# Performance work log

Measured on AMD Instinct MI355X. Metric: run time of the kernel, lower is better.

## Reference

```python
import jax, jax.numpy as jnp
import numpy as np

NT, NH, NW = 16, 16, 16
HEADS, DIM_HEAD = 8, 64
DIM = 512
DEPTH = 4
EPS = 1e-5


def _layernorm(x, g, b):
    mu = jnp.mean(x, axis=-1, keepdims=True)
    var = jnp.mean(jnp.square(x - mu), axis=-1, keepdims=True)
    return (x - mu) * jax.lax.rsqrt(var + EPS) * g + b


def setup_inputs() -> dict:
    key = jax.random.key(0)
    ks = jax.random.split(key, 4)
    n = NT * NH * NW
    inner = HEADS * DIM_HEAD
    x = jax.random.normal(ks[0], (8, n, DIM), dtype=jnp.float32)
    Wqkv = jax.random.normal(ks[1], (DEPTH, DIM, 3 * inner), dtype=jnp.float32) * (DIM ** -0.5)
    Wout = jax.random.normal(ks[2], (DEPTH, inner, DIM), dtype=jnp.float32) * (inner ** -0.5)
    bout = jnp.zeros((DEPTH, DIM), dtype=jnp.float32)
    gamma = jnp.ones((DEPTH, DIM), dtype=jnp.float32)
    beta = jnp.zeros((DEPTH, DIM), dtype=jnp.float32)
    return {"x": x, "Wqkv": Wqkv, "Wout": Wout, "bout": bout, "gamma": gamma, "beta": beta}


def _fda_layer(x, Wqkv, Wout, bout, g, bb):
    b, n, d = x.shape
    hs = HEADS // 2
    s = NH * NW
    scale = DIM_HEAD ** -0.5
    y = _layernorm(x, g, bb)
    qkv = y @ Wqkv  # (b, n, 3*inner)
    q, k, v = jnp.split(qkv, 3, axis=-1)
    # b n (h d) -> b h n d
    def to_heads(t):
        return t.reshape(b, n, HEADS, DIM_HEAD).transpose(0, 2, 1, 3)
    q, k, v = to_heads(q), to_heads(k), to_heads(v)
    # spatial branch: first half of heads, view n as (t, s)
    qs = q[:, :hs].reshape(b, hs, NT, s, DIM_HEAD)
    ks = k[:, :hs].reshape(b, hs, NT, s, DIM_HEAD)
    vs = v[:, :hs].reshape(b, hs, NT, s, DIM_HEAD)
    sp_dots = jnp.einsum('bhtid,bhtjd->bhtij', qs, ks) * scale
    sp_attn = jax.nn.softmax(sp_dots, axis=-1)
    sp_out = jnp.einsum('bhtij,bhtjd->bhtid', sp_attn, vs)  # (b,hs,nt,s,dh)
    # temporal branch: second half of heads, view n as (s, t)
    qt = q[:, hs:].reshape(b, hs, s, NT, DIM_HEAD)
    kt = k[:, hs:].reshape(b, hs, s, NT, DIM_HEAD)
    vt = v[:, hs:].reshape(b, hs, s, NT, DIM_HEAD)
    tp_dots = jnp.einsum('bhsid,bhsjd->bhsij', qt, kt) * scale
    tp_attn = jax.nn.softmax(tp_dots, axis=-1)
    tp_out = jnp.einsum('bhsij,bhsjd->bhsid', tp_attn, vt)  # (b,hs,s,nt,dh)
    out = jnp.concatenate([sp_out.reshape(b, hs, n, DIM_HEAD),
                           tp_out.reshape(b, hs, n, DIM_HEAD)], axis=1)  # (b,h,n,dh)
    out = out.transpose(0, 2, 1, 3).reshape(b, n, HEADS * DIM_HEAD)
    return out @ Wout + bout


def reference(x, Wqkv, Wout, bout, gamma, beta):
    for l in range(DEPTH):
        x = _fda_layer(x, Wqkv[l], Wout[l], bout[l], gamma[l], beta[l]) + x
    return x
```

## Files before the change

kernel.cpp:

```cpp
#include <hip/hip_runtime.h>
#include <hip/hip_bf16.h>

typedef __bf16 bf16x8 __attribute__((ext_vector_type(8)));
typedef float f32x4 __attribute__((ext_vector_type(4)));

#define AS1(p) ((const __attribute__((address_space(1))) void*)(p))
#define AS3(p) ((__attribute__((address_space(3))) void*)(p))

__global__ __launch_bounds__(256) void transpose32(const float* __restrict__ W,
                                                   __bf16* __restrict__ WT,
                                                   int K, int N) {
  __shared__ float t[32][33];
  int l = blockIdx.z;
  int k0 = blockIdx.y * 32, n0 = blockIdx.x * 32;
  int tx = threadIdx.x & 31, ty = threadIdx.x >> 5;
  const float* src = W + ((size_t)l * K + k0) * N + n0;
#pragma unroll
  for (int i = 0; i < 32; i += 8) t[ty + i][tx] = src[(size_t)(ty + i) * N + tx];
  __syncthreads();
  __bf16* dst = WT + ((size_t)l * N + n0) * K + k0;
#pragma unroll
  for (int i = 0; i < 32; i += 8) dst[(size_t)(ty + i) * K + tx] = (__bf16)t[tx][ty + i];
}

__global__ __launch_bounds__(256) void ln_kernel(const float* __restrict__ x,
                                                 const float* __restrict__ gamma,
                                                 const float* __restrict__ beta,
                                                 __bf16* __restrict__ y) {
  int wave = threadIdx.x >> 6, lane = threadIdx.x & 63;
  size_t row = (size_t)blockIdx.x * 4 + wave;
  const float* xr = x + row * 512 + lane * 8;
  float4 v0 = *(const float4*)xr;
  float4 v1 = *(const float4*)(xr + 4);
  float s = v0.x + v0.y + v0.z + v0.w + v1.x + v1.y + v1.z + v1.w;
  float ss = v0.x * v0.x + v0.y * v0.y + v0.z * v0.z + v0.w * v0.w +
             v1.x * v1.x + v1.y * v1.y + v1.z * v1.z + v1.w * v1.w;
#pragma unroll
  for (int m = 1; m < 64; m <<= 1) {
    s += __shfl_xor(s, m);
    ss += __shfl_xor(ss, m);
  }
  float mean = s * (1.f / 512.f);
  float var = ss * (1.f / 512.f) - mean * mean;
  float rstd = rsqrtf(var + 1e-5f);
  const float* gp = gamma + lane * 8;
  const float* bp = beta + lane * 8;
  float4 g0 = *(const float4*)gp, g1 = *(const float4*)(gp + 4);
  float4 b0 = *(const float4*)bp, b1 = *(const float4*)(bp + 4);
  bf16x8 o;
  o[0] = (__bf16)((v0.x - mean) * rstd * g0.x + b0.x);
  o[1] = (__bf16)((v0.y - mean) * rstd * g0.y + b0.y);
  o[2] = (__bf16)((v0.z - mean) * rstd * g0.z + b0.z);
  o[3] = (__bf16)((v0.w - mean) * rstd * g0.w + b0.w);
  o[4] = (__bf16)((v1.x - mean) * rstd * g1.x + b1.x);
  o[5] = (__bf16)((v1.y - mean) * rstd * g1.y + b1.y);
  o[6] = (__bf16)((v1.z - mean) * rstd * g1.z + b1.z);
  o[7] = (__bf16)((v1.w - mean) * rstd * g1.w + b1.w);
  *(bf16x8*)(y + row * 512 + lane * 8) = o;
}

#define STAGE_PART(kt_, part_)                                                   \
  {                                                                              \
    const __bf16* gb_ = ((part_) < 2) ? Abase : Bbase;                           \
    int rowoff_ = ((part_)&1) * 128;                                             \
    const __bf16* g0_ = gb_ + (size_t)(rowoff_ + r0s) * 512 + (kt_)*64 + s0 * 8; \
    const __bf16* g1_ = gb_ + (size_t)(rowoff_ + r1s) * 512 + (kt_)*64 + s1 * 8; \
    char* lb_ = lds + (((kt_)&1) * 65536) + ((part_)*16384);                     \
    __builtin_amdgcn_global_load_lds(AS1(g0_), AS3(lb_ + ldsw0), 16, 0, 0);      \
    __builtin_amdgcn_global_load_lds(AS1(g1_), AS3(lb_ + ldsw1), 16, 0, 0);      \
  }

template <int NCOLS>
__global__ __launch_bounds__(512, 2) void gemm256(const __bf16* __restrict__ A,
                                                  const __bf16* __restrict__ BT,
                                                  __bf16* __restrict__ Cb) {
  extern __shared__ __attribute__((aligned(128))) char lds[];
  constexpr int NT = NCOLS / 256;
  int bid = blockIdx.x;
  int cpx = gridDim.x >> 3;
  int L = (bid & 7) * cpx + (bid >> 3);
  int tileM = L / NT, tileN = L - tileM * NT;
  int tid = threadIdx.x;
  int l = tid & 63, w = tid >> 6;
  int lm = l & 15, lh = l >> 4;
  int wave_m = w >> 2, wave_n = w & 3;
  const __bf16* Abase = A + (size_t)tileM * 256 * 512;
  const __bf16* Bbase = BT + (size_t)tileN * 256 * 512;
  int r0s = tid >> 3, s0 = (tid & 7) ^ (r0s & 7);
  int p1 = tid + 512;
  int r1s = p1 >> 3, s1 = (p1 & 7) ^ (r1s & 7);
  int ldsw0 = (w * 64) * 16, ldsw1 = (512 + w * 64) * 16;

  f32x4 acc[8][4];
#pragma unroll
  for (int m = 0; m < 8; ++m)
#pragma unroll
    for (int n = 0; n < 4; ++n) acc[m][n] = (f32x4){0.f, 0.f, 0.f, 0.f};

  int xorv = (lm & 7) << 4;
  int kb0 = (lh * 16) ^ xorv;
  int kb1 = (64 + lh * 16) ^ xorv;
  int arow = wave_m * 128 + lm;
  int brow = wave_n * 64 + lm;

  STAGE_PART(0, 0); STAGE_PART(0, 1); STAGE_PART(0, 2); STAGE_PART(0, 3);

  for (int kt = 0; kt < 8; ++kt) {
    char* sb = lds + (kt & 1) * 65536;
    if (kt < 7) {
      STAGE_PART(kt + 1, 0);
      asm volatile("s_waitcnt vmcnt(2)" ::: "memory");
    } else {
      asm volatile("s_waitcnt vmcnt(0)" ::: "memory");
    }
    __builtin_amdgcn_sched_barrier(0);
    __builtin_amdgcn_s_barrier();
    bf16x8 bfrag[4][2];
#pragma unroll
    for (int nf = 0; nf < 4; ++nf) {
      const char* bp = sb + 32768 + (brow + nf * 16) * 128;
      bfrag[nf][0] = *(const bf16x8*)(bp + kb0);
      bfrag[nf][1] = *(const bf16x8*)(bp + kb1);
    }
#pragma unroll
    for (int ph = 0; ph < 4; ++ph) {
      bf16x8 af[2][2];
#pragma unroll
      for (int m = 0; m < 2; ++m) {
        const char* ap = sb + (arow + (ph * 2 + m) * 16) * 128;
        af[m][0] = *(const bf16x8*)(ap + kb0);
        af[m][1] = *(const bf16x8*)(ap + kb1);
      }
      if (ph == 0 && kt < 7) STAGE_PART(kt + 1, 1);
      if (ph == 1 && kt < 7) STAGE_PART(kt + 1, 2);
      if (ph == 2 && kt < 7) STAGE_PART(kt + 1, 3);
      __builtin_amdgcn_s_setprio(1);
#pragma unroll
      for (int m = 0; m < 2; ++m)
#pragma unroll
        for (int nf = 0; nf < 4; ++nf) {
          acc[ph * 2 + m][nf] = __builtin_amdgcn_mfma_f32_16x16x32_bf16(
              af[m][0], bfrag[nf][0], acc[ph * 2 + m][nf], 0, 0, 0);
          acc[ph * 2 + m][nf] = __builtin_amdgcn_mfma_f32_16x16x32_bf16(
              af[m][1], bfrag[nf][1], acc[ph * 2 + m][nf], 0, 0, 0);
        }
      __builtin_amdgcn_s_setprio(0);
    }
    __builtin_amdgcn_s_barrier();
  }

  __syncthreads();
  __bf16* lw = (__bf16*)(lds + w * 9216);
  int crow0 = tileM * 256 + wave_m * 128;
  int ccol = tileN * 256 + wave_n * 64 + (l & 7) * 8;
#pragma unroll
  for (int half = 0; half < 2; ++half) {
#pragma unroll
    for (int m2 = 0; m2 < 4; ++m2) {
      int mf = half * 4 + m2;
#pragma unroll
      for (int nf = 0; nf < 4; ++nf)
#pragma unroll
        for (int r = 0; r < 4; ++r)
          lw[(m2 * 16 + lh * 4 + r) * 72 + nf * 16 + lm] = (__bf16)acc[mf][nf][r];
    }
    asm volatile("s_waitcnt lgkmcnt(0)" ::: "memory");
    __builtin_amdgcn_sched_barrier(0);
#pragma unroll
    for (int p = 0; p < 8; ++p) {
      int lrow = p * 8 + (l >> 3);
      bf16x8 v = *(const bf16x8*)&lw[lrow * 72 + (l & 7) * 8];
      *(bf16x8*)&Cb[(size_t)(crow0 + half * 64 + lrow) * NCOLS + ccol] = v;
    }
    asm volatile("s_waitcnt lgkmcnt(0)" ::: "memory");
    __builtin_amdgcn_sched_barrier(0);
  }
}

#define STAGE_SB(kt_)                                                            \
  {                                                                              \
    const __bf16* gA0_ = Abase + (size_t)rA0 * 512 + (kt_)*64 + sA0 * 8;         \
    const __bf16* gA1_ = Abase + (size_t)rA1 * 512 + (kt_)*64 + sA1 * 8;         \
    __builtin_amdgcn_global_load_lds(AS1(gA0_), AS3(lds + dW0), 16, 0, 0);       \
    __builtin_amdgcn_global_load_lds(AS1(gA1_), AS3(lds + 8192 + dW0), 16, 0, 0);\
    __builtin_amdgcn_global_load_lds(AS1(Bbase + (size_t)rA0 * 512 + (kt_)*64 + sA0 * 8), \
                                     AS3(lds + 16384 + dW0), 16, 0, 0);          \
    __builtin_amdgcn_global_load_lds(AS1(Bbase + (size_t)rA1 * 512 + (kt_)*64 + sA1 * 8), \
                                     AS3(lds + 24576 + dW0), 16, 0, 0);          \
    __builtin_amdgcn_global_load_lds(AS1(Bbase + (size_t)(128 + rA0) * 512 + (kt_)*64 + sA0 * 8), \
                                     AS3(lds + 32768 + dW0), 16, 0, 0);          \
    __builtin_amdgcn_global_load_lds(AS1(Bbase + (size_t)(128 + rA1) * 512 + (kt_)*64 + sA1 * 8), \
                                     AS3(lds + 40960 + dW0), 16, 0, 0);          \
  }

__global__ __launch_bounds__(512) void gemm_sb(const __bf16* __restrict__ A,
                                               const __bf16* __restrict__ BT,
                                               __bf16* __restrict__ Cb) {
  extern __shared__ __attribute__((aligned(128))) char lds[];
  constexpr int NCOLS = 1536;
  constexpr int NT = 6;
  int bid = blockIdx.x;
  int cpx = gridDim.x >> 3;
  int L = (bid & 7) * cpx + (bid >> 3);
  int tileM = L / NT, tileN = L - tileM * NT;
  int tid = threadIdx.x;
  int l = tid & 63, w = tid >> 6;
  int lm = l & 15, lh = l >> 4;
  int wave_m = w >> 2, wave_n = w & 3;
  const __bf16* Abase = A + (size_t)tileM * 128 * 512;
  const __bf16* Bbase = BT + (size_t)tileN * 256 * 512;
  int rA0 = tid >> 3, sA0 = (tid & 7) ^ (rA0 & 7);
  int p1 = tid + 512;
  int rA1 = p1 >> 3, sA1 = (p1 & 7) ^ (rA1 & 7);
  int dW0 = w * 1024;

  f32x4 acc[4][4];
#pragma unroll
  for (int m = 0; m < 4; ++m)
#pragma unroll
    for (int n = 0; n < 4; ++n) acc[m][n] = (f32x4){0.f, 0.f, 0.f, 0.f};

  int xorv = (lm & 7) << 4;
  int kb0 = (lh * 16) ^ xorv;
  int kb1 = (64 + lh * 16) ^ xorv;
  int arow = wave_m * 64 + lm;
  int brow = wave_n * 64 + lm;

  STAGE_SB(0);
  asm volatile("s_waitcnt vmcnt(0)" ::: "memory");
  __builtin_amdgcn_sched_barrier(0);
  __builtin_amdgcn_s_barrier();

  for (int kt = 0; kt < 8; ++kt) {
    bf16x8 bfrag[4][2];
#pragma unroll
    for (int nf = 0; nf < 4; ++nf) {
      const char* bp = lds + 16384 + (brow + nf * 16) * 128;
      bfrag[nf][0] = *(const bf16x8*)(bp + kb0);
      bfrag[nf][1] = *(const bf16x8*)(bp + kb1);
    }
    __builtin_amdgcn_s_setprio(1);
#pragma unroll
    for (int mf = 0; mf < 4; ++mf) {
      const char* ap = lds + (arow + mf * 16) * 128;
      bf16x8 af0 = *(const bf16x8*)(ap + kb0);
      bf16x8 af1 = *(const bf16x8*)(ap + kb1);
#pragma unroll
      for (int nf = 0; nf < 4; ++nf) {
        acc[mf][nf] = __builtin_amdgcn_mfma_f32_16x16x32_bf16(af0, bfrag[nf][0],
                                                              acc[mf][nf], 0, 0, 0);
        acc[mf][nf] = __builtin_amdgcn_mfma_f32_16x16x32_bf16(af1, bfrag[nf][1],
                                                              acc[mf][nf], 0, 0, 0);
      }
    }
    __builtin_amdgcn_s_setprio(0);
    asm volatile("s_waitcnt lgkmcnt(0)" ::: "memory");
    __builtin_amdgcn_sched_barrier(0);
    __builtin_amdgcn_s_barrier();
    if (kt < 7) {
      STAGE_SB(kt + 1);
      asm volatile("s_waitcnt vmcnt(0)" ::: "memory");
      __builtin_amdgcn_sched_barrier(0);
      __builtin_amdgcn_s_barrier();
    }
  }

  __syncthreads();
  __bf16* lw = (__bf16*)(lds + w * 4608);
  int crow0 = tileM * 128 + wave_m * 64;
  int ccol = tileN * 256 + wave_n * 64 + (l & 7) * 8;
#pragma unroll
  for (int half = 0; half < 2; ++half) {
#pragma unroll
    for (int m2 = 0; m2 < 2; ++m2) {
      int mf = half * 2 + m2;
#pragma unroll
      for (int nf = 0; nf < 4; ++nf)
#pragma unroll
        for (int r = 0; r < 4; ++r)
          lw[(m2 * 16 + lh * 4 + r) * 72 + nf * 16 + lm] = (__bf16)acc[mf][nf][r];
    }
    asm volatile("s_waitcnt lgkmcnt(0)" ::: "memory");
    __builtin_amdgcn_sched_barrier(0);
#pragma unroll
    for (int p = 0; p < 4; ++p) {
      int lrow = p * 8 + (l >> 3);
      bf16x8 v = *(const bf16x8*)&lw[lrow * 72 + (l & 7) * 8];
      *(bf16x8*)&Cb[(size_t)(crow0 + half * 32 + lrow) * NCOLS + ccol] = v;
    }
    asm volatile("s_waitcnt lgkmcnt(0)" ::: "memory");
    __builtin_amdgcn_sched_barrier(0);
  }
}

#define STAGE128(kt_, part_)                                                    \
  {                                                                             \
    const __bf16* gb_ = ((part_) == 0) ? Abase : Bbase;                         \
    const __bf16* g0_ = gb_ + (size_t)r0s * 512 + (kt_)*64 + s0 * 8;            \
    const __bf16* g1_ = gb_ + (size_t)r1s * 512 + (kt_)*64 + s1 * 8;            \
    char* lb_ = lds + (((kt_)&1) * 32768) + ((part_)*16384);                    \
    __builtin_amdgcn_global_load_lds(AS1(g0_), AS3(lb_ + ldsw0), 16, 0, 0);     \
    __builtin_amdgcn_global_load_lds(AS1(g1_), AS3(lb_ + ldsw1), 16, 0, 0);     \
  }

__global__ __launch_bounds__(512, 4) void gemm128res(const __bf16* __restrict__ A,
                                                     const __bf16* __restrict__ BT,
                                                     float* Cf,
                                                     const float* __restrict__ bias,
                                                     const float* Resid) {
  extern __shared__ __attribute__((aligned(128))) char lds[];
  constexpr int NCOLS = 512;
  constexpr int NT = 4;
  int bid = blockIdx.x;
  int cpx = gridDim.x >> 3;
  int L = (bid & 7) * cpx + (bid >> 3);
  int tileM = L / NT, tileN = L - tileM * NT;
  int tid = threadIdx.x;
  int l = tid & 63, w = tid >> 6;
  int lm = l & 15, lh = l >> 4;
  int wave_m = w >> 2, wave_n = w & 3;
  const __bf16* Abase = A + (size_t)tileM * 128 * 512;
  const __bf16* Bbase = BT + (size_t)tileN * 128 * 512;
  int r0s = tid >> 3, s0 = (tid & 7) ^ (r0s & 7);
  int p1 = tid + 512;
  int r1s = p1 >> 3, s1 = (p1 & 7) ^ (r1s & 7);
  int ldsw0 = (w * 64) * 16, ldsw1 = 8192 + (w * 64) * 16;

  f32x4 acc[4][2];
#pragma unroll
  for (int m = 0; m < 4; ++m)
#pragma unroll
    for (int n = 0; n < 2; ++n) acc[m][n] = (f32x4){0.f, 0.f, 0.f, 0.f};

  int xorv = (lm & 7) << 4;
  int kb0 = (lh * 16) ^ xorv;
  int kb1 = (64 + lh * 16) ^ xorv;
  int arow = wave_m * 64 + lm;
  int brow = wave_n * 32 + lm;

  STAGE128(0, 0); STAGE128(0, 1);

  for (int kt = 0; kt < 8; ++kt) {
    char* sb = lds + (kt & 1) * 32768;
    if (kt < 7) {
      STAGE128(kt + 1, 0);
      asm volatile("s_waitcnt vmcnt(2)" ::: "memory");
    } else {
      asm volatile("s_waitcnt vmcnt(0)" ::: "memory");
    }
    __builtin_amdgcn_sched_barrier(0);
    __builtin_amdgcn_s_barrier();
    bf16x8 bfrag[2][2];
#pragma unroll
    for (int nf = 0; nf < 2; ++nf) {
      const char* bp = sb + 16384 + (brow + nf * 16) * 128;
      bfrag[nf][0] = *(const bf16x8*)(bp + kb0);
      bfrag[nf][1] = *(const bf16x8*)(bp + kb1);
    }
    bf16x8 af[4][2];
#pragma unroll
    for (int mf = 0; mf < 4; ++mf) {
      const char* ap = sb + (arow + mf * 16) * 128;
      af[mf][0] = *(const bf16x8*)(ap + kb0);
      af[mf][1] = *(const bf16x8*)(ap + kb1);
    }
    if (kt < 7) STAGE128(kt + 1, 1);
    __builtin_amdgcn_s_setprio(1);
#pragma unroll
    for (int mf = 0; mf < 4; ++mf)
#pragma unroll
      for (int nf = 0; nf < 2; ++nf) {
        acc[mf][nf] = __builtin_amdgcn_mfma_f32_16x16x32_bf16(af[mf][0], bfrag[nf][0],
                                                              acc[mf][nf], 0, 0, 0);
        acc[mf][nf] = __builtin_amdgcn_mfma_f32_16x16x32_bf16(af[mf][1], bfrag[nf][1],
                                                              acc[mf][nf], 0, 0, 0);
      }
    __builtin_amdgcn_s_setprio(0);
    __builtin_amdgcn_s_barrier();
  }

  float* lf = (float*)(lds + w * 2560);
  int crow0 = tileM * 128 + wave_m * 64;
  int ccol0 = tileN * 128 + wave_n * 32;
  int erow = l >> 2;
  int ecl = (l & 3) * 8;
  float4 ba = *(const float4*)(bias + ccol0 + ecl);
  float4 bb = *(const float4*)(bias + ccol0 + ecl + 4);
#pragma unroll
  for (int mf = 0; mf < 4; ++mf) {
#pragma unroll
    for (int nf = 0; nf < 2; ++nf)
#pragma unroll
      for (int r = 0; r < 4; ++r)
        lf[(lh * 4 + r) * 40 + nf * 16 + lm] = acc[mf][nf][r];
    size_t rowg = (size_t)(crow0 + mf * 16 + erow);
    const float* rp = Resid + rowg * NCOLS + ccol0 + ecl;
    float* cp = Cf + rowg * NCOLS + ccol0 + ecl;
    float4 a0 = *(float4*)&lf[erow * 40 + ecl];
    float4 a1 = *(float4*)&lf[erow * 40 + ecl + 4];
    float4 r0 = *(const float4*)rp;
    float4 r1 = *(const float4*)(rp + 4);
    float4 o0, o1;
    o0.x = a0.x + ba.x + r0.x; o0.y = a0.y + ba.y + r0.y;
    o0.z = a0.z + ba.z + r0.z; o0.w = a0.w + ba.w + r0.w;
    o1.x = a1.x + bb.x + r1.x; o1.y = a1.y + bb.y + r1.y;
    o1.z = a1.z + bb.z + r1.z; o1.w = a1.w + bb.w + r1.w;
    *(float4*)cp = o0;
    *(float4*)(cp + 4) = o1;
  }
}

__global__ __launch_bounds__(256) void attn_spatial(const __bf16* __restrict__ qkv,
                                                    __bf16* __restrict__ attn_out) {
  __shared__ __attribute__((aligned(16))) __bf16 VT[64 * 256];
  __shared__ __attribute__((aligned(16))) __bf16 P[4][4096];
  int bid = blockIdx.x;
  int b = bid >> 6;
  int rem = bid & 63;
  int h = rem >> 4;
  int t = rem & 15;
  int tid = threadIdx.x;
  int w = tid >> 6, l = tid & 63;
  size_t nbase = (size_t)b * 4096 + t * 256;
#pragma unroll
  for (int i = 0; i < 8; i++) {
    int idx = tid + i * 256;
    int key = idx >> 3, dseg = idx & 7;
    bf16x8 v = *(const bf16x8*)(qkv + (nbase + key) * 1536 + 1024 + h * 64 + dseg * 8);
#pragma unroll
    for (int d2 = 0; d2 < 8; d2++) {
      int dh = dseg * 8 + d2;
      VT[dh * 256 + (((key >> 3) ^ (dh & 7)) << 3) + (key & 7)] = v[d2];
    }
  }
  __syncthreads();
  int lm = l & 15, lh = l >> 4;
  for (int it = 0; it < 4; ++it) {
    int qbase = it * 64 + w * 16;
    const __bf16* qp = qkv + (nbase + qbase + lm) * 1536 + h * 64 + lh * 8;
    bf16x8 aq0 = *(const bf16x8*)qp;
    bf16x8 aq1 = *(const bf16x8*)(qp + 32);
    f32x4 sa[16];
#pragma unroll
    for (int tn = 0; tn < 16; ++tn) {
      const __bf16* kp = qkv + (nbase + tn * 16 + lm) * 1536 + 512 + h * 64 + lh * 8;
      bf16x8 bk0 = *(const bf16x8*)kp;
      bf16x8 bk1 = *(const bf16x8*)(kp + 32);
      f32x4 z = {0.f, 0.f, 0.f, 0.f};
      z = __builtin_amdgcn_mfma_f32_16x16x32_bf16(aq0, bk0, z, 0, 0, 0);
      sa[tn] = __builtin_amdgcn_mfma_f32_16x16x32_bf16(aq1, bk1, z, 0, 0, 0);
    }
    float rmax[4] = {-1e30f, -1e30f, -1e30f, -1e30f};
#pragma unroll
    for (int tn = 0; tn < 16; ++tn)
#pragma unroll
      for (int r = 0; r < 4; ++r) {
        sa[tn][r] *= 0.125f;
        rmax[r] = fmaxf(rmax[r], sa[tn][r]);
      }
#pragma unroll
    for (int m = 1; m < 16; m <<= 1)
#pragma unroll
      for (int r = 0; r < 4; ++r) rmax[r] = fmaxf(rmax[r], __shfl_xor(rmax[r], m));
    float rsum[4] = {0.f, 0.f, 0.f, 0.f};
#pragma unroll
    for (int tn = 0; tn < 16; ++tn)
#pragma unroll
      for (int r = 0; r < 4; ++r) {
        float e = __expf(sa[tn][r] - rmax[r]);
        sa[tn][r] = e;
        rsum[r] += e;
      }
#pragma unroll
    for (int m = 1; m < 16; m <<= 1)
#pragma unroll
      for (int r = 0; r < 4; ++r) rsum[r] += __shfl_xor(rsum[r], m);
    float rinv[4];
#pragma unroll
    for (int r = 0; r < 4; ++r) rinv[r] = 1.f / rsum[r];
#pragma unroll
    for (int tn = 0; tn < 16; ++tn)
#pragma unroll
      for (int r = 0; r < 4; ++r) {
        int row = lh * 4 + r;
        int col = tn * 16 + lm;
        P[w][row * 256 + ((((col >> 3)) ^ (row & 7)) << 3) + (col & 7)] =
            (__bf16)(sa[tn][r] * rinv[r]);
      }
    f32x4 oa[4];
#pragma unroll
    for (int nt = 0; nt < 4; ++nt) oa[nt] = (f32x4){0.f, 0.f, 0.f, 0.f};
#pragma unroll
    for (int kc = 0; kc < 8; ++kc) {
      bf16x8 pa = *(const bf16x8*)&P[w][lm * 256 + (((kc * 4 + lh) ^ (lm & 7)) << 3)];
#pragma unroll
      for (int nt = 0; nt < 4; ++nt) {
        int dh = nt * 16 + lm;
        bf16x8 bv = *(const bf16x8*)&VT[dh * 256 + (((kc * 4 + lh) ^ (dh & 7)) << 3)];
        oa[nt] = __builtin_amdgcn_mfma_f32_16x16x32_bf16(pa, bv, oa[nt], 0, 0, 0);
      }
    }
#pragma unroll
    for (int nt = 0; nt < 4; ++nt)
#pragma unroll
      for (int r = 0; r < 4; ++r) {
        size_t row = nbase + qbase + lh * 4 + r;
        attn_out[row * 512 + h * 64 + nt * 16 + lm] = (__bf16)oa[nt][r];
      }
  }
}

__global__ __launch_bounds__(256) void attn_temporal(const __bf16* __restrict__ qkv,
                                                     __bf16* __restrict__ attn_out) {
  __shared__ __attribute__((aligned(16))) __bf16 VT[4][64 * 40];
  __shared__ __attribute__((aligned(16))) __bf16 P[4][16 * 40];
  int tid = threadIdx.x;
  {
    float4 z4 = {0.f, 0.f, 0.f, 0.f};
#pragma unroll
    for (int i = 0; i < 5; ++i) ((float4*)&VT[0][0])[tid + i * 256] = z4;
    if (tid < 64) ((float4*)&P[0][0])[tid + 256] = z4;
    ((float4*)&P[0][0])[tid] = z4;
  }
  __syncthreads();
  int bid = blockIdx.x;
  int b = bid >> 8;
  int rem = bid & 255;
  int h = 4 + (rem >> 6);
  int g = rem & 63;
  int w = tid >> 6, l = tid & 63;
  int lm = l & 15, lh = l >> 4;
  int sid = g * 4 + w;
  size_t n0 = (size_t)b * 4096 + sid * 16;

  const __bf16* qp = qkv + (n0 + lm) * 1536 + h * 64 + lh * 8;
  bf16x8 aq0 = *(const bf16x8*)qp;
  bf16x8 aq1 = *(const bf16x8*)(qp + 32);
  const __bf16* kp = qp + 512;
  bf16x8 bk0 = *(const bf16x8*)kp;
  bf16x8 bk1 = *(const bf16x8*)(kp + 32);
  int kk = l >> 2;
  int dh0 = (l & 3) * 8;
  const __bf16* vp = qkv + (n0 + kk) * 1536 + 1024 + h * 64 + dh0;
  bf16x8 vr0 = *(const bf16x8*)vp;
  bf16x8 vr1 = *(const bf16x8*)(vp + 32);

  f32x4 s4 = {0.f, 0.f, 0.f, 0.f};
  s4 = __builtin_amdgcn_mfma_f32_16x16x32_bf16(aq0, bk0, s4, 0, 0, 0);
  s4 = __builtin_amdgcn_mfma_f32_16x16x32_bf16(aq1, bk1, s4, 0, 0, 0);

#pragma unroll
  for (int d2 = 0; d2 < 8; ++d2) VT[w][(dh0 + d2) * 40 + kk] = vr0[d2];
#pragma unroll
  for (int d2 = 0; d2 < 8; ++d2) VT[w][(dh0 + 32 + d2) * 40 + kk] = vr1[d2];

  float e[4];
  float rmax[4];
#pragma unroll
  for (int r = 0; r < 4; ++r) {
    e[r] = s4[r] * 0.125f;
    rmax[r] = e[r];
  }
#pragma unroll
  for (int m = 1; m < 16; m <<= 1)
#pragma unroll
    for (int r = 0; r < 4; ++r) rmax[r] = fmaxf(rmax[r], __shfl_xor(rmax[r], m));
  float rsum[4];
#pragma unroll
  for (int r = 0; r < 4; ++r) {
    e[r] = __expf(e[r] - rmax[r]);
    rsum[r] = e[r];
  }
#pragma unroll
  for (int m = 1; m < 16; m <<= 1)
#pragma unroll
    for (int r = 0; r < 4; ++r) rsum[r] += __shfl_xor(rsum[r], m);
#pragma unroll
  for (int r = 0; r < 4; ++r)
    P[w][(lh * 4 + r) * 40 + lm] = (__bf16)(e[r] / rsum[r]);

  asm volatile("s_waitcnt lgkmcnt(0)" ::: "memory");
  __builtin_amdgcn_sched_barrier(0);

  bf16x8 pa = *(const bf16x8*)&P[w][lm * 40 + lh * 8];
#pragma unroll
  for (int nt = 0; nt < 4; ++nt) {
    bf16x8 bv = *(const bf16x8*)&VT[w][(nt * 16 + lm) * 40 + lh * 8];
    f32x4 oa = {0.f, 0.f, 0.f, 0.f};
    oa = __builtin_amdgcn_mfma_f32_16x16x32_bf16(pa, bv, oa, 0, 0, 0);
#pragma unroll
    for (int r = 0; r < 4; ++r)
      attn_out[(n0 + lh * 4 + r) * 512 + h * 64 + nt * 16 + lm] = (__bf16)oa[r];
  }
}

extern "C" void kernel_launch(void* const* d_in, const int* in_sizes, int n_in,
                              void* d_out, int out_size, void* d_ws, size_t ws_size,
                              hipStream_t stream) {
  const float* x = (const float*)d_in[0];
  const float* Wqkv = (const float*)d_in[1];
  const float* Wout = (const float*)d_in[2];
  const float* bout = (const float*)d_in[3];
  const float* gamma = (const float*)d_in[4];
  const float* beta = (const float*)d_in[5];
  float* out = (float*)d_out;

  const size_t OFF_WOUT = 6291456;
  const size_t OFF_Y = OFF_WOUT + 2097152;
  const size_t OFF_QKV = OFF_Y + 33554432;
  const size_t NEEDED = OFF_QKV + 100663296;
  if (ws_size < NEEDED) return;
  char* ws = (char*)d_ws;
  __bf16* WqkvT = (__bf16*)ws;
  __bf16* WoutT = (__bf16*)(ws + OFF_WOUT);
  __bf16* ybuf = (__bf16*)(ws + OFF_Y);
  __bf16* qkv = (__bf16*)(ws + OFF_QKV);

  hipFuncSetAttribute((const void*)gemm256<1536>,
                      hipFuncAttributeMaxDynamicSharedMemorySize, 131072);
  hipFuncSetAttribute((const void*)gemm_sb,
                      hipFuncAttributeMaxDynamicSharedMemorySize, 49152);
  hipFuncSetAttribute((const void*)gemm128res,
                      hipFuncAttributeMaxDynamicSharedMemorySize, 65536);

  transpose32<<<dim3(48, 16, 4), 256, 0, stream>>>(Wqkv, WqkvT, 512, 1536);
  transpose32<<<dim3(16, 16, 4), 256, 0, stream>>>(Wout, WoutT, 512, 512);

  for (int layer = 0; layer < 4; ++layer) {
    const float* src = (layer == 0) ? x : out;
    ln_kernel<<<8192, 256, 0, stream>>>(src, gamma + layer * 512, beta + layer * 512, ybuf);
    if (layer & 1) {
      gemm_sb<<<1536, 512, 49152, stream>>>(
          ybuf, WqkvT + (size_t)layer * 1536 * 512, qkv);
    } else {
      gemm256<1536><<<768, 512, 131072, stream>>>(
          ybuf, WqkvT + (size_t)layer * 1536 * 512, qkv);
    }
    attn_spatial<<<512, 256, 0, stream>>>(qkv, ybuf);
    attn_temporal<<<2048, 256, 0, stream>>>(qkv, ybuf);
    gemm128res<<<1024, 512, 65536, stream>>>(
        ybuf, WoutT + (size_t)layer * 512 * 512, out, bout + layer * 512, src);
  }
}
```

Before: 647.4 us.

## Double-buffer QKV GEMM LDS stages with K=32 steps to overlap loads

Reworks the gemm_sb QKV projection kernel, used on odd layers, from a single-buffered K=64 stage into a double-buffered K=32 pipeline in the same 48KB of LDS. The next tile's global-to-LDS loads are issued before computing on the current one, with a partial vmcnt wait. This hides global load latency behind MFMA work instead of stalling on a full wait each iteration. In exchange it runs twice as many iterations with barriers and uses a new XOR swizzle for the narrower 64-byte rows, which may cause LDS bank conflicts.

```diff
diff --git a/kernel.cpp b/kernel.cpp
--- a/kernel.cpp
+++ b/kernel.cpp
@@ -177,25 +177,22 @@
   }
 }
 
-#define STAGE_SB(kt_)                                                            \
+#define STAGE_SB2(kt_)                                                           \
   {                                                                              \
-    const __bf16* gA0_ = Abase + (size_t)rA0 * 512 + (kt_)*64 + sA0 * 8;         \
-    const __bf16* gA1_ = Abase + (size_t)rA1 * 512 + (kt_)*64 + sA1 * 8;         \
-    __builtin_amdgcn_global_load_lds(AS1(gA0_), AS3(lds + dW0), 16, 0, 0);       \
-    __builtin_amdgcn_global_load_lds(AS1(gA1_), AS3(lds + 8192 + dW0), 16, 0, 0);\
-    __builtin_amdgcn_global_load_lds(AS1(Bbase + (size_t)rA0 * 512 + (kt_)*64 + sA0 * 8), \
-                                     AS3(lds + 16384 + dW0), 16, 0, 0);          \
-    __builtin_amdgcn_global_load_lds(AS1(Bbase + (size_t)rA1 * 512 + (kt_)*64 + sA1 * 8), \
-                                     AS3(lds + 24576 + dW0), 16, 0, 0);          \
-    __builtin_amdgcn_global_load_lds(AS1(Bbase + (size_t)(128 + rA0) * 512 + (kt_)*64 + sA0 * 8), \
-                                     AS3(lds + 32768 + dW0), 16, 0, 0);          \
-    __builtin_amdgcn_global_load_lds(AS1(Bbase + (size_t)(128 + rA1) * 512 + (kt_)*64 + sA1 * 8), \
-                                     AS3(lds + 40960 + dW0), 16, 0, 0);          \
-  }
-
-__global__ __launch_bounds__(512) void gemm_sb(const __bf16* __restrict__ A,
-                                               const __bf16* __restrict__ BT,
-                                               __bf16* __restrict__ Cb) {
+    char* lb_ = lds + (((kt_)&1) * 24576);                                       \
+    __builtin_amdgcn_global_load_lds(                                            \
+        AS1(Abase + (size_t)rS * 512 + (kt_)*32 + sS * 8), AS3(lb_ + dW), 16, 0, 0); \
+    __builtin_amdgcn_global_load_lds(                                            \
+        AS1(Bbase + (size_t)rS * 512 + (kt_)*32 + sS * 8),                       \
+        AS3(lb_ + 8192 + dW), 16, 0, 0);                                         \
+    __builtin_amdgcn_global_load_lds(                                            \
+        AS1(Bbase + (size_t)(128 + rS) * 512 + (kt_)*32 + sS * 8),               \
+        AS3(lb_ + 16384 + dW), 16, 0, 0);                                        \
+  }
+
+__global__ __launch_bounds__(512) void gemm_sb2(const __bf16* __restrict__ A,
+                                                const __bf16* __restrict__ BT,
+                                                __bf16* __restrict__ Cb) {
   extern __shared__ __attribute__((aligned(128))) char lds[];
   constexpr int NCOLS = 1536;
   constexpr int NT = 6;
@@ -209,10 +206,9 @@
   int wave_m = w >> 2, wave_n = w & 3;
   const __bf16* Abase = A + (size_t)tileM * 128 * 512;
   const __bf16* Bbase = BT + (size_t)tileN * 256 * 512;
-  int rA0 = tid >> 3, sA0 = (tid & 7) ^ (rA0 & 7);
-  int p1 = tid + 512;
-  int rA1 = p1 >> 3, sA1 = (p1 & 7) ^ (rA1 & 7);
-  int dW0 = w * 1024;
+  int rS = tid >> 2;
+  int sS = (tid & 3) ^ ((tid >> 3) & 3);
+  int dW = w * 1024;
 
   f32x4 acc[4][4];
 #pragma unroll
@@ -220,49 +216,39 @@
 #pragma unroll
     for (int n = 0; n < 4; ++n) acc[m][n] = (f32x4){0.f, 0.f, 0.f, 0.f};
 
-  int xorv = (lm & 7) << 4;
-  int kb0 = (lh * 16) ^ xorv;
-  int kb1 = (64 + lh * 16) ^ xorv;
+  int kb = (lh ^ ((lm >> 1) & 3)) << 4;
   int arow = wave_m * 64 + lm;
   int brow = wave_n * 64 + lm;
 
-  STAGE_SB(0);
-  asm volatile("s_waitcnt vmcnt(0)" ::: "memory");
-  __builtin_amdgcn_sched_barrier(0);
-  __builtin_amdgcn_s_barrier();
-
-  for (int kt = 0; kt < 8; ++kt) {
-    bf16x8 bfrag[4][2];
-#pragma unroll
-    for (int nf = 0; nf < 4; ++nf) {
-      const char* bp = lds + 16384 + (brow + nf * 16) * 128;
-      bfrag[nf][0] = *(const bf16x8*)(bp + kb0);
-      bfrag[nf][1] = *(const bf16x8*)(bp + kb1);
-    }
-    __builtin_amdgcn_s_setprio(1);
-#pragma unroll
-    for (int mf = 0; mf < 4; ++mf) {
-      const char* ap = lds + (arow + mf * 16) * 128;
-      bf16x8 af0 = *(const bf16x8*)(ap + kb0);
-      bf16x8 af1 = *(const bf16x8*)(ap + kb1);
-#pragma unroll
-      for (int nf = 0; nf < 4; ++nf) {
-        acc[mf][nf] = __builtin_amdgcn_mfma_f32_16x16x32_bf16(af0, bfrag[nf][0],
-                                                              acc[mf][nf], 0, 0, 0);
-        acc[mf][nf] = __builtin_amdgcn_mfma_f32_16x16x32_bf16(af1, bfrag[nf][1],
-                                                              acc[mf][nf], 0, 0, 0);
-      }
-    }
-    __builtin_amdgcn_s_setprio(0);
-    asm volatile("s_waitcnt lgkmcnt(0)" ::: "memory");
+  STAGE_SB2(0);
+
+  for (int kt = 0; kt < 16; ++kt) {
+    const char* sb = lds + (kt & 1) * 24576;
+    if (kt < 15) {
+      STAGE_SB2(kt + 1);
+      asm volatile("s_waitcnt vmcnt(3)" ::: "memory");
+    } else {
+      asm volatile("s_waitcnt vmcnt(0)" ::: "memory");
+    }
     __builtin_amdgcn_sched_barrier(0);
     __builtin_amdgcn_s_barrier();
-    if (kt < 7) {
-      STAGE_SB(kt + 1);
-      asm volatile("s_waitcnt vmcnt(0)" ::: "memory");
-      __builtin_amdgcn_sched_barrier(0);
-      __builtin_amdgcn_s_barrier();
-    }
+    bf16x8 bfrag[4];
+#pragma unroll
+    for (int nf = 0; nf < 4; ++nf)
+      bfrag[nf] = *(const bf16x8*)(sb + 8192 + (brow + nf * 16) * 64 + kb);
+    bf16x8 af[4];
+#pragma unroll
+    for (int mf = 0; mf < 4; ++mf)
+      af[mf] = *(const bf16x8*)(sb + (arow + mf * 16) * 64 + kb);
+    __builtin_amdgcn_s_setprio(1);
+#pragma unroll
+    for (int mf = 0; mf < 4; ++mf)
+#pragma unroll
+      for (int nf = 0; nf < 4; ++nf)
+        acc[mf][nf] = __builtin_amdgcn_mfma_f32_16x16x32_bf16(af[mf], bfrag[nf],
+                                                              acc[mf][nf], 0, 0, 0);
+    __builtin_amdgcn_s_setprio(0);
+    __builtin_amdgcn_s_barrier();
   }
 
   __syncthreads();
@@ -618,7 +604,7 @@
 
   hipFuncSetAttribute((const void*)gemm256<1536>,
                       hipFuncAttributeMaxDynamicSharedMemorySize, 131072);
-  hipFuncSetAttribute((const void*)gemm_sb,
+  hipFuncSetAttribute((const void*)gemm_sb2,
                       hipFuncAttributeMaxDynamicSharedMemorySize, 49152);
   hipFuncSetAttribute((const void*)gemm128res,
                       hipFuncAttributeMaxDynamicSharedMemorySize, 65536);
@@ -630,7 +616,7 @@
     const float* src = (layer == 0) ? x : out;
     ln_kernel<<<8192, 256, 0, stream>>>(src, gamma + layer * 512, beta + layer * 512, ybuf);
     if (layer & 1) {
-      gemm_sb<<<1536, 512, 49152, stream>>>(
+      gemm_sb2<<<1536, 512, 49152, stream>>>(
           ybuf, WqkvT + (size_t)layer * 1536 * 512, qkv);
     } else {
       gemm256<1536><<<768, 512, 131072, stream>>>(
```

Measured after the change: 658.5 us. About the same (+1.7%).
